# Performance work log

Measured on AMD Instinct MI355X. Metric: run time of the kernel, lower is better.

Reference implementation:

```python
import jax, jax.numpy as jnp
import numpy as np

B, M, L, D = 64, 128, 20, 1024


def setup_inputs() -> dict:
    key = jax.random.key(0)
    ks = jax.random.split(key, 16)
    s = 0.05  # weight scale to keep LSTM gates out of saturation
    rn = lambda k, shape: jax.random.normal(k, shape, jnp.float32) * s
    return {
        'encoder_out': jax.random.normal(ks[0], (B, M + 1, D), jnp.float32),
        'obj_seq': jax.random.randint(ks[1], (B, L), 0, M),
        'att_mask': jnp.ones((B, M + 1), jnp.int32),
        'bos_w': rn(ks[2], (1, D)),
        'eos_w': rn(ks[3], (1, D)),
        'Wp': rn(ks[4], (D, D)), 'bp': jnp.zeros((D,), jnp.float32),
        'Wih1': rn(ks[5], (4 * D, 3 * D)), 'Whh1': rn(ks[6], (4 * D, D)),
        'bih1': jnp.zeros((4 * D,), jnp.float32), 'bhh1': jnp.zeros((4 * D,), jnp.float32),
        'Wih2': rn(ks[7], (4 * D, 2 * D)), 'Whh2': rn(ks[8], (4 * D, D)),
        'bih2': jnp.zeros((4 * D,), jnp.float32), 'bhh2': jnp.zeros((4 * D,), jnp.float32),
        'Wah': rn(ks[9], (D, D)), 'bah': jnp.zeros((D,), jnp.float32),
        'wa': rn(ks[10], (D,)), 'ba': jnp.zeros((1,), jnp.float32),
        'Wae': rn(ks[11], (D, D)), 'bae': jnp.zeros((D,), jnp.float32),
        'Woe': rn(ks[12], (D, D)), 'boe': jnp.zeros((D,), jnp.float32),
    }


def _lstm_cell(x, h, c, Wih, Whh, bih, bhh):
    # torch LSTMCell gate order: i, f, g, o
    g = x @ Wih.T + bih + h @ Whh.T + bhh
    i, f, gg, o = jnp.split(g, 4, axis=-1)
    c_new = jax.nn.sigmoid(f) * c + jax.nn.sigmoid(i) * jnp.tanh(gg)
    h_new = jax.nn.sigmoid(o) * jnp.tanh(c_new)
    return h_new, c_new


def _forward(encoder_out, obj_seq, att_mask, bos_w, eos_w, Wp, bp,
             Wih1, Whh1, bih1, bhh1, Wih2, Whh2, bih2, bhh2,
             Wah, bah, wa, ba, Wae, bae, Woe, boe):
    b, _, d = encoder_out.shape
    gv = encoder_out[:, 0, :]                      # [B, D]
    att_feats = encoder_out[:, 1:, :]              # [B, M, D]
    idx = jnp.broadcast_to(obj_seq[:, :, None], obj_seq.shape + (d,)).astype(jnp.int32)
    obj_feat = jnp.take_along_axis(att_feats, idx, axis=1)          # [B, L, D]
    bos = jnp.broadcast_to(bos_w, (b, 1, d))
    obj_feat = jnp.concatenate([bos, obj_feat], axis=1)             # [B, L+1, D]
    p_att = att_feats @ Wp.T + bp                  # [B, M, D]
    amask = att_mask[:, 1:]                        # [B, M]

    def attend(h1):
        dot = jnp.tanh(p_att + (h1 @ Wah.T + bah)[:, None, :])      # [B, M, D]
        score = dot @ wa + ba[0]                                    # [B, M]
        score = jnp.where(amask == 0, -1e9, score)
        alpha = jax.nn.softmax(score, axis=-1)
        return jnp.einsum('bm,bmd->bd', alpha, att_feats)

    def step(carry, x_t):
        h1, c1, h2, c2 = carry
        inp1 = jnp.concatenate([h2, gv, x_t], axis=-1)              # [B, 3D]
        h1, c1 = _lstm_cell(inp1, h1, c1, Wih1, Whh1, bih1, bhh1)
        att = attend(h1)
        inp2 = jnp.concatenate([att, h1], axis=-1)                  # [B, 2D]
        h2, c2 = _lstm_cell(inp2, h2, c2, Wih2, Whh2, bih2, bhh2)
        return (h1, c1, h2, c2), h2

    z = jnp.zeros((b, d), encoder_out.dtype)
    _, outs = jax.lax.scan(step, (z, z, z, z), jnp.swapaxes(obj_feat, 0, 1))
    outputs = jnp.swapaxes(outs, 0, 1)             # [B, L+1, D]

    # NCE branch (cfg.LOSSES.NCE.STOP_GRAD = True)
    nce_att = jax.lax.stop_gradient(att_feats)
    afe = nce_att @ Wae.T + bae
    eos = jnp.broadcast_to(eos_w, (b, 1, d))
    afe = jnp.concatenate([eos, afe], axis=1)      # [B, M+1, D]
    ofe = outputs @ Woe.T + boe                    # [B, L+1, D]
    nce_logit = jnp.einsum('bld,bmd->blm', ofe, afe)  # [B, L+1, M+1]
    return outputs, nce_logit


def reference(encoder_out, obj_seq, att_mask, bos_w, eos_w, Wp, bp,
              Wih1, Whh1, bih1, bhh1, Wih2, Whh2, bih2, bhh2,
              Wah, bah, wa, ba, Wae, bae, Woe, boe):
    return _forward(encoder_out, obj_seq, att_mask, bos_w, eos_w, Wp, bp,
                    Wih1, Whh1, bih1, bhh1, Wih2, Whh2, bih2, bhh2,
                    Wah, bah, wa, ba, Wae, bae, Woe, boe)
```

## Files before the change

### kernel.cpp

```cpp
#include <hip/hip_runtime.h>
#include <cmath>

typedef unsigned short u16;
typedef __attribute__((ext_vector_type(8))) short short8;
typedef __attribute__((ext_vector_type(4))) float floatx4;
typedef __attribute__((address_space(3))) unsigned int lds_u32;
typedef const __attribute__((address_space(1))) unsigned int glob_u32;

__device__ __forceinline__ u16 f2bf(float f) {
    unsigned u = __float_as_uint(f);
    unsigned r = u + 0x7fffu + ((u >> 16) & 1u);
    return (u16)(r >> 16);
}
__device__ __forceinline__ float bf2f(u16 h) { return __uint_as_float(((unsigned)h) << 16); }
__device__ __forceinline__ void split2(float x, u16& hi, u16& lo) {
    hi = f2bf(x);
    lo = f2bf(x - bf2f(hi));
}
__device__ __forceinline__ float sigm(float x) {
    x = fminf(fmaxf(x, -30.f), 30.f);
    return 1.0f / (1.0f + __expf(-x));
}
__device__ __forceinline__ float ftanh(float x) {
    x = fminf(fmaxf(x, -15.f), 15.f);
    float e = __expf(2.f * x);
    return (e - 1.f) / (e + 1.f);
}
__device__ __forceinline__ void gload16(const void* g, void* l) {
    __builtin_amdgcn_global_load_lds((glob_u32*)g, (lds_u32*)l, 16, 0, 0);
}

__global__ __launch_bounds__(256) void k_cvt(const float* __restrict__ s, u16* __restrict__ d, int n4) {
    int i = blockIdx.x * 256 + threadIdx.x;
    int stride = gridDim.x * 256;
    for (; i < n4; i += stride) {
        float4 v = ((const float4*)s)[i];
        ushort4 o;
        o.x = f2bf(v.x); o.y = f2bf(v.y); o.z = f2bf(v.z); o.w = f2bf(v.w);
        ((ushort4*)d)[i] = o;
    }
}

__global__ __launch_bounds__(256) void k_cvt_att(const float* __restrict__ enc, u16* __restrict__ dst) {
    int m = blockIdx.x, b = blockIdx.y, tid = threadIdx.x;
    const float* src = enc + ((size_t)b * 129 + 1 + m) * 1024;
    float4 v = *(const float4*)(src + tid * 4);
    ushort4 o;
    o.x = f2bf(v.x); o.y = f2bf(v.y); o.z = f2bf(v.z); o.w = f2bf(v.w);
    *(ushort4*)(dst + ((size_t)b * 128 + m) * 1024 + tid * 4) = o;
}

__global__ __launch_bounds__(256) void k_splitp(const float* __restrict__ s, u16* __restrict__ hi,
                                                u16* __restrict__ lo, int n4) {
    int i = blockIdx.x * 256 + threadIdx.x;
    int stride = gridDim.x * 256;
    for (; i < n4; i += stride) {
        float4 v = ((const float4*)s)[i];
        ushort4 h, l;
        split2(v.x, h.x, l.x); split2(v.y, h.y, l.y);
        split2(v.z, h.z, l.z); split2(v.w, h.w, l.w);
        ((ushort4*)hi)[i] = h;
        ((ushort4*)lo)[i] = l;
    }
}

__global__ __launch_bounds__(256) void k_build_w1cat(const float* __restrict__ Wih1, const float* __restrict__ Whh1,
                                                     u16* __restrict__ dh, u16* __restrict__ dl) {
    int row = blockIdx.x;
    int c = threadIdx.x * 8;
    const float* src = (c < 1024) ? (Wih1 + (size_t)row * 3072 + c) : (Whh1 + (size_t)row * 1024 + (c - 1024));
    short8 h, l;
#pragma unroll
    for (int j = 0; j < 8; ++j) { u16 hh, ll; split2(src[j], hh, ll); h[j] = (short)hh; l[j] = (short)ll; }
    *(short8*)(dh + (size_t)row * 2048 + c) = h;
    *(short8*)(dl + (size_t)row * 2048 + c) = l;
}

__global__ __launch_bounds__(384) void k_build_wcat2(const float* __restrict__ Wih2, const float* __restrict__ Whh2,
                                                     u16* __restrict__ dh, u16* __restrict__ dl) {
    int row = blockIdx.x;
    int c = threadIdx.x * 8;
    const float* src = (c < 2048) ? (Wih2 + (size_t)row * 2048 + c) : (Whh2 + (size_t)row * 1024 + (c - 2048));
    short8 h, l;
#pragma unroll
    for (int j = 0; j < 8; ++j) { u16 hh, ll; split2(src[j], hh, ll); h[j] = (short)hh; l[j] = (short)ll; }
    *(short8*)(dh + (size_t)row * 3072 + c) = h;
    *(short8*)(dl + (size_t)row * 3072 + c) = l;
}

__global__ __launch_bounds__(256) void k_build_wx1(const float* __restrict__ Wih1, u16* __restrict__ dh,
                                                   u16* __restrict__ dl) {
    int row = blockIdx.x;
    int c = threadIdx.x * 8;
    const float* src = Wih1 + (size_t)row * 3072 + 1024 + c;
    short8 h, l;
#pragma unroll
    for (int j = 0; j < 8; ++j) { u16 hh, ll; split2(src[j], hh, ll); h[j] = (short)hh; l[j] = (short)ll; }
    *(short8*)(dh + (size_t)row * 2048 + c) = h;
    *(short8*)(dl + (size_t)row * 2048 + c) = l;
}

__global__ __launch_bounds__(256) void k_build_xaug(const float* __restrict__ enc, const int* __restrict__ obj,
                                                    const float* __restrict__ bos_w, u16* __restrict__ dh,
                                                    u16* __restrict__ dl) {
    int b = blockIdx.x, t = blockIdx.y, tid = threadIdx.x;
    const float* gv = enc + (size_t)b * 129 * 1024;
    const float* xr;
    if (t == 0) xr = bos_w;
    else {
        int idx = obj[b * 20 + (t - 1)];
        idx = min(max(idx, 0), 127);
        xr = enc + ((size_t)b * 129 + 1 + idx) * 1024;
    }
    size_t rowoff = ((size_t)b * 21 + t) * 2048;
    float4 v0 = *(const float4*)(gv + tid * 4);
    float4 v1 = *(const float4*)(xr + tid * 4);
    ushort4 h0, l0, h1, l1;
    split2(v0.x, h0.x, l0.x); split2(v0.y, h0.y, l0.y); split2(v0.z, h0.z, l0.z); split2(v0.w, h0.w, l0.w);
    split2(v1.x, h1.x, l1.x); split2(v1.y, h1.y, l1.y); split2(v1.z, h1.z, l1.z); split2(v1.w, h1.w, l1.w);
    *(ushort4*)(dh + rowoff + tid * 4) = h0;
    *(ushort4*)(dl + rowoff + tid * 4) = l0;
    *(ushort4*)(dh + rowoff + 1024 + tid * 4) = h1;
    *(ushort4*)(dl + rowoff + 1024 + tid * 4) = l1;
}

template <int APASS, int BPASS, int AREMAP, bool BF16OUT>
__global__ __launch_bounds__(256)
void k_gemm3(const u16* __restrict__ Ah, const u16* __restrict__ Al, int lda,
             const u16* __restrict__ Wh, const u16* __restrict__ Wl, int ldw,
             const float* __restrict__ b1, const float* __restrict__ b2,
             void* __restrict__ Cout, int ldc, int Mrows, int K) {
    constexpr int NP = APASS + BPASS;
    __shared__ char lds[2][NP][8192];
    const int tid = threadIdx.x;
    const int lane = tid & 63;
    const int lr = lane & 15, lk = lane >> 4;
    const int m0 = blockIdx.y * 128, n0 = blockIdx.x * 128;
    const int wid = tid >> 6;
    const int wr = wid >> 1, wc = wid & 1;
    const int wbyte = (tid & 192) * 16;

    floatx4 acc[4][4] = {};
    const int nt = K >> 5;

    auto stage = [&](int bb, int kt) {
        int k0 = kt * 32;
#pragma unroll
        for (int i = 0; i < 2; ++i) {
            int p = i * 256 + tid;
            int s = p ^ ((p >> 2) & 3);
            int row = s >> 2, kc = s & 3;
            size_t aoff;
            int gm = m0 + row;
            if (AREMAP == 1) aoff = (((size_t)(gm >> 7)) * 129 + 1 + (gm & 127)) * 1024 + k0 + kc * 8;
            else {
                int cm = gm < Mrows ? gm : Mrows - 1;
                aoff = (size_t)cm * lda + k0 + kc * 8;
            }
            gload16(Ah + aoff, &lds[bb][0][i * 4096 + wbyte]);
            if constexpr (APASS == 2) gload16(Al + aoff, &lds[bb][1][i * 4096 + wbyte]);
            size_t woff = (size_t)(n0 + row) * ldw + k0 + kc * 8;
            gload16(Wh + woff, &lds[bb][APASS][i * 4096 + wbyte]);
            if constexpr (BPASS == 2) gload16(Wl + woff, &lds[bb][APASS + 1][i * 4096 + wbyte]);
        }
    };

    stage(0, 0);
    __syncthreads();
    for (int t = 0; t < nt; ++t) {
        int bb = t & 1;
        if (t + 1 < nt) stage(bb ^ 1, t + 1);
        short8 ah_[4], al_[4], bh_[4], bl_[4];
#pragma unroll
        for (int mi = 0; mi < 4; ++mi) {
            int row = wr * 64 + mi * 16 + lr;
            int slot = (row * 4 + (lk ^ (row & 3))) * 16;
            ah_[mi] = *(const short8*)&lds[bb][0][slot];
            if constexpr (APASS == 2) al_[mi] = *(const short8*)&lds[bb][1][slot];
        }
#pragma unroll
        for (int ni = 0; ni < 4; ++ni) {
            int row = wc * 64 + ni * 16 + lr;
            int slot = (row * 4 + (lk ^ (row & 3))) * 16;
            bh_[ni] = *(const short8*)&lds[bb][APASS][slot];
            if constexpr (BPASS == 2) bl_[ni] = *(const short8*)&lds[bb][APASS + 1][slot];
        }
#pragma unroll
        for (int mi = 0; mi < 4; ++mi)
#pragma unroll
            for (int ni = 0; ni < 4; ++ni) {
                acc[mi][ni] = __builtin_amdgcn_mfma_f32_16x16x32_bf16(ah_[mi], bh_[ni], acc[mi][ni], 0, 0, 0);
                if constexpr (BPASS == 2)
                    acc[mi][ni] = __builtin_amdgcn_mfma_f32_16x16x32_bf16(ah_[mi], bl_[ni], acc[mi][ni], 0, 0, 0);
                if constexpr (APASS == 2)
                    acc[mi][ni] = __builtin_amdgcn_mfma_f32_16x16x32_bf16(al_[mi], bh_[ni], acc[mi][ni], 0, 0, 0);
            }
        __syncthreads();
    }
#pragma unroll
    for (int mi = 0; mi < 4; ++mi) {
#pragma unroll
        for (int r = 0; r < 4; ++r) {
            int gm = m0 + wr * 64 + mi * 16 + lk * 4 + r;
            if (AREMAP == 0 && gm >= Mrows) continue;
#pragma unroll
            for (int ni = 0; ni < 4; ++ni) {
                int gn = n0 + wc * 64 + ni * 16 + lr;
                float v = acc[mi][ni][r];
                if (b1) v += b1[gn];
                if (b2) v += b2[gn];
                if (BF16OUT) ((u16*)Cout)[(size_t)gm * ldc + gn] = f2bf(v);
                else ((float*)Cout)[(size_t)gm * ldc + gn] = v;
            }
        }
    }
}

__global__ __launch_bounds__(256)
void k_gp3(const u16* __restrict__ Xh, const u16* __restrict__ Xl, int ldx,
           const u16* __restrict__ Wh, const u16* __restrict__ Wl, int ldw,
           int Klen, float* __restrict__ P, int Ntot) {
    __shared__ char lds[2][4][4096];
    const int tid = threadIdx.x, wid = tid >> 6, lane = tid & 63;
    const int lr = lane & 15, lk = lane >> 4;
    const int n0 = blockIdx.x * 64;
    const int koff = blockIdx.y * Klen;
    floatx4 acc[4] = {};
    const int nt = Klen >> 5;
    const int wbyte = (tid & 192) * 16;
    const int srow = tid >> 2, skc = (tid & 3) ^ (srow & 3);
    const size_t xoff = (size_t)srow * ldx + skc * 8;
    const size_t woff = (size_t)(n0 + srow) * ldw + skc * 8;

    auto stage = [&](int bb, int kt) {
        int k0 = koff + kt * 32;
        gload16(Xh + xoff + k0, &lds[bb][0][wbyte]);
        gload16(Xl + xoff + k0, &lds[bb][1][wbyte]);
        gload16(Wh + woff + k0, &lds[bb][2][wbyte]);
        gload16(Wl + woff + k0, &lds[bb][3][wbyte]);
    };

    stage(0, 0);
    __syncthreads();
    for (int t = 0; t < nt; ++t) {
        int bb = t & 1;
        if (t + 1 < nt) stage(bb ^ 1, t + 1);
        int arow = wid * 16 + lr;
        int aslot = (arow * 4 + (lk ^ (arow & 3))) * 16;
        short8 xh = *(const short8*)&lds[bb][0][aslot];
        short8 xl = *(const short8*)&lds[bb][1][aslot];
#pragma unroll
        for (int ni = 0; ni < 4; ++ni) {
            int brow = ni * 16 + lr;
            int bslot = (brow * 4 + (lk ^ (brow & 3))) * 16;
            short8 wh = *(const short8*)&lds[bb][2][bslot];
            short8 wl = *(const short8*)&lds[bb][3][bslot];
            acc[ni] = __builtin_amdgcn_mfma_f32_16x16x32_bf16(xh, wh, acc[ni], 0, 0, 0);
            acc[ni] = __builtin_amdgcn_mfma_f32_16x16x32_bf16(xh, wl, acc[ni], 0, 0, 0);
            acc[ni] = __builtin_amdgcn_mfma_f32_16x16x32_bf16(xl, wh, acc[ni], 0, 0, 0);
        }
        __syncthreads();
    }
    float* Pb = P + (size_t)blockIdx.y * 64 * Ntot;
#pragma unroll
    for (int ni = 0; ni < 4; ++ni)
#pragma unroll
        for (int r = 0; r < 4; ++r) {
            int b = wid * 16 + lk * 4 + r;
            Pb[(size_t)b * Ntot + n0 + ni * 16 + lr] = acc[ni][r];
        }
}

__global__ __launch_bounds__(256)
void k_finish(const float* __restrict__ P, int Ntot, int nP, const float* __restrict__ xcf,
              const float* __restrict__ b1, const float* __restrict__ b2,
              float* __restrict__ cst,
              u16* __restrict__ w1h, u16* __restrict__ w1l, int w1s,
              u16* __restrict__ w2h, u16* __restrict__ w2l, int w2s,
              float* __restrict__ outf, u16* __restrict__ oh) {
    int idx = blockIdx.x * 256 + threadIdx.x;
    int b = idx >> 10, d = idx & 1023;
    float g[4];
#pragma unroll
    for (int q = 0; q < 4; ++q) {
        int n = q * 1024 + d;
        float s = 0.f;
        for (int p = 0; p < nP; ++p) s += P[((size_t)p * 64 + b) * Ntot + n];
        if (xcf) s += xcf[(size_t)b * 21 * 4096 + n];
        if (b1) s += b1[n];
        if (b2) s += b2[n];
        g[q] = s;
    }
    float cp = cst[idx];
    float cn = sigm(g[1]) * cp + sigm(g[0]) * ftanh(g[2]);
    float hn = sigm(g[3]) * ftanh(cn);
    cst[idx] = cn;
    u16 hh, hl;
    split2(hn, hh, hl);
    w1h[b * w1s + d] = hh; w1l[b * w1s + d] = hl;
    w2h[b * w2s + d] = hh; w2l[b * w2s + d] = hl;
    if (outf) outf[(size_t)b * 21 * 1024 + d] = hn;
    if (oh) oh[(size_t)b * 21 * 1024 + d] = hh;
}

__global__ __launch_bounds__(256)
void k_score(const float* __restrict__ PAH, const float* __restrict__ bah,
             const float* __restrict__ wa, const float* __restrict__ ba,
             const u16* __restrict__ Patt, const int* __restrict__ amask, float* __restrict__ SC) {
    int mc = blockIdx.x, b = blockIdx.y, tid = threadIdx.x;
    __shared__ float sah[1024], swa[1024];
    {
        int d = tid * 4;
        *(float4*)&swa[d] = *(const float4*)(wa + d);
        float4 s;
        float* sp = &s.x;
#pragma unroll
        for (int j = 0; j < 4; ++j) {
            float acc = bah[d + j];
#pragma unroll
            for (int p = 0; p < 4; ++p) acc += PAH[((size_t)p * 64 + b) * 1024 + d + j];
            sp[j] = acc;
        }
        *(float4*)&sah[d] = s;
    }
    __syncthreads();
    int wv = tid >> 6, lane = tid & 63;
    float bav = ba[0];
    for (int j = 0; j < 8; ++j) {
        int m = mc * 32 + wv * 8 + j;
        const u16* pr = Patt + ((size_t)(b * 128 + m)) * 1024;
        float part = 0.f;
#pragma unroll
        for (int c = 0; c < 4; ++c) {
            int d = c * 256 + lane * 4;
            ushort4 p4 = *(const ushort4*)(pr + d);
            float4 a4 = *(const float4*)&sah[d];
            float4 w4 = *(const float4*)&swa[d];
            part += ftanh(bf2f(p4.x) + a4.x) * w4.x + ftanh(bf2f(p4.y) + a4.y) * w4.y +
                    ftanh(bf2f(p4.z) + a4.z) * w4.z + ftanh(bf2f(p4.w) + a4.w) * w4.w;
        }
#pragma unroll
        for (int off = 32; off; off >>= 1) part += __shfl_down(part, off, 64);
        if (lane == 0) {
            float sc = part + bav;
            if (amask[b * 129 + 1 + m] == 0) sc = -1e9f;
            SC[b * 128 + m] = sc;
        }
    }
}

__global__ __launch_bounds__(256)
void k_attsum(const float* __restrict__ SC, const u16* __restrict__ attf,
              u16* __restrict__ X2h, u16* __restrict__ X2l) {
    int dc = blockIdx.x, b = blockIdx.y, tid = threadIdx.x;
    __shared__ float salpha[128];
    __shared__ float sred[8];
    float sv = (tid < 128) ? SC[b * 128 + tid] : -1e30f;
    float mx = sv;
#pragma unroll
    for (int off = 32; off; off >>= 1) mx = fmaxf(mx, __shfl_down(mx, off, 64));
    if ((tid & 63) == 0) sred[tid >> 6] = mx;
    __syncthreads();
    float gmx = fmaxf(fmaxf(sred[0], sred[1]), fmaxf(sred[2], sred[3]));
    float ev = (tid < 128) ? __expf(sv - gmx) : 0.f;
    float s = ev;
#pragma unroll
    for (int off = 32; off; off >>= 1) s += __shfl_down(s, off, 64);
    if ((tid & 63) == 0) sred[4 + (tid >> 6)] = s;
    __syncthreads();
    float gsum = sred[4] + sred[5] + sred[6] + sred[7];
    if (tid < 128) salpha[tid] = ev / gsum;
    __syncthreads();
    int d = dc * 256 + tid;
    const u16* base = attf + (size_t)b * 128 * 1024 + d;
    float acc = 0.f;
#pragma unroll 8
    for (int m = 0; m < 128; ++m) acc += salpha[m] * bf2f(base[(size_t)m * 1024]);
    u16 hh, hl;
    split2(acc, hh, hl);
    X2h[b * 3072 + d] = hh;
    X2l[b * 3072 + d] = hl;
}

__global__ __launch_bounds__(256)
void k_nce(const float* __restrict__ OFE, const float* __restrict__ AFE,
           const float* __restrict__ eos_w, float* __restrict__ nce) {
    int l = blockIdx.x, b = blockIdx.y;
    __shared__ float sofe[1024];
    int tid = threadIdx.x;
    {
        float4 v = *(const float4*)(OFE + ((size_t)b * 21 + l) * 1024 + tid * 4);
        *(float4*)&sofe[tid * 4] = v;
    }
    __syncthreads();
    int w = tid >> 6, lane = tid & 63;
    float* outp = nce + ((size_t)b * 21 + l) * 129;
    for (int j = w; j < 129; j += 4) {
        const float* ar = (j == 0) ? eos_w : AFE + ((size_t)b * 128 + (j - 1)) * 1024;
        float part = 0.f;
#pragma unroll
        for (int c = 0; c < 4; ++c) {
            float4 a4 = *(const float4*)(ar + c * 256 + lane * 4);
            float4 o4 = *(const float4*)&sofe[c * 256 + lane * 4];
            part += a4.x * o4.x + a4.y * o4.y + a4.z * o4.z + a4.w * o4.w;
        }
#pragma unroll
        for (int off = 32; off; off >>= 1) part += __shfl_down(part, off, 64);
        if (lane == 0) outp[j] = part;
    }
}

extern "C" void kernel_launch(void* const* d_in, const int* in_sizes, int n_in,
                              void* d_out, int out_size, void* d_ws, size_t ws_size,
                              hipStream_t stream) {
    const float* enc  = (const float*)d_in[0];
    const int*   obj  = (const int*)d_in[1];
    const int*   amask= (const int*)d_in[2];
    const float* bosw = (const float*)d_in[3];
    const float* eosw = (const float*)d_in[4];
    const float* Wp   = (const float*)d_in[5];
    const float* bp   = (const float*)d_in[6];
    const float* Wih1 = (const float*)d_in[7];
    const float* Whh1 = (const float*)d_in[8];
    const float* bih1 = (const float*)d_in[9];
    const float* bhh1 = (const float*)d_in[10];
    const float* Wih2 = (const float*)d_in[11];
    const float* Whh2 = (const float*)d_in[12];
    const float* bih2 = (const float*)d_in[13];
    const float* bhh2 = (const float*)d_in[14];
    const float* Wah  = (const float*)d_in[15];
    const float* bah  = (const float*)d_in[16];
    const float* wa   = (const float*)d_in[17];
    const float* ba   = (const float*)d_in[18];
    const float* Wae  = (const float*)d_in[19];
    const float* bae  = (const float*)d_in[20];
    const float* Woe  = (const float*)d_in[21];
    const float* boe  = (const float*)d_in[22];

    float* outputs = (float*)d_out;
    float* nce     = outputs + (size_t)64 * 21 * 1024;

    char* wp = (char*)d_ws;
    auto alloc = [&](size_t bytes) -> char* { char* p = wp; wp += (bytes + 255) & ~(size_t)255; return p; };
    u16* encbf  = (u16*)alloc((size_t)64 * 129 * 1024 * 2);
    u16* Wph    = (u16*)alloc((size_t)1024 * 1024 * 2);
    u16* Wpl    = (u16*)alloc((size_t)1024 * 1024 * 2);
    u16* Xaugh  = (u16*)alloc((size_t)1344 * 2048 * 2);
    u16* Xaugl  = (u16*)alloc((size_t)1344 * 2048 * 2);
    u16* W1h    = (u16*)alloc((size_t)4096 * 2048 * 2);
    u16* W1l    = (u16*)alloc((size_t)4096 * 2048 * 2);
    u16* W2h    = (u16*)alloc((size_t)4096 * 3072 * 2);
    u16* W2l    = (u16*)alloc((size_t)4096 * 3072 * 2);
    u16* Wahh   = (u16*)alloc((size_t)1024 * 1024 * 2);
    u16* Wahl   = (u16*)alloc((size_t)1024 * 1024 * 2);
    u16* Waeh   = (u16*)alloc((size_t)1024 * 1024 * 2);
    u16* Wael   = (u16*)alloc((size_t)1024 * 1024 * 2);
    u16* Woeh   = (u16*)alloc((size_t)1024 * 1024 * 2);
    u16* Woel   = (u16*)alloc((size_t)1024 * 1024 * 2);
    char* region1 = alloc((size_t)2 * 4096 * 2048 * 2);
    u16* Wx1h = (u16*)region1;
    u16* Wx1l = (u16*)region1 + (size_t)4096 * 2048;
    float* AFE32 = (float*)region1;
    u16* PattBf  = (u16*)alloc((size_t)8192 * 1024 * 2);
    u16* attfbf  = (u16*)alloc((size_t)64 * 128 * 1024 * 2);
    float* Xcf   = (float*)alloc((size_t)1344 * 4096 * 4);
    u16* Xouth   = (u16*)alloc((size_t)1344 * 1024 * 2);
    float* P2    = (float*)alloc((size_t)8 * 64 * 4096 * 4);
    float* OFE32 = (float*)Xaugh;
    char* sp2 = (char*)encbf;
    auto alloc2 = [&](size_t bytes) -> char* { char* p = sp2; sp2 += (bytes + 255) & ~(size_t)255; return p; };
    float* P1  = (float*)alloc2((size_t)8 * 64 * 4096 * 4);
    float* PAH = (float*)alloc2((size_t)4 * 64 * 1024 * 4);
    u16* XHh   = (u16*)alloc2((size_t)64 * 2048 * 2);
    u16* XHl   = (u16*)alloc2((size_t)64 * 2048 * 2);
    u16* X2h   = (u16*)alloc2((size_t)64 * 3072 * 2);
    u16* X2l   = (u16*)alloc2((size_t)64 * 3072 * 2);
    float* c1  = (float*)alloc2((size_t)64 * 1024 * 4);
    float* c2  = (float*)alloc2((size_t)64 * 1024 * 4);
    float* SC  = (float*)alloc2((size_t)64 * 128 * 4);

    dim3 blk(256);
    k_cvt<<<2048, blk, 0, stream>>>(enc, encbf, 64 * 129 * 1024 / 4);
    k_cvt_att<<<dim3(128, 64), blk, 0, stream>>>(enc, attfbf);
    k_splitp<<<1024, blk, 0, stream>>>(Wp, Wph, Wpl, 1024 * 1024 / 4);
    k_splitp<<<1024, blk, 0, stream>>>(Wah, Wahh, Wahl, 1024 * 1024 / 4);
    k_splitp<<<1024, blk, 0, stream>>>(Wae, Waeh, Wael, 1024 * 1024 / 4);
    k_splitp<<<1024, blk, 0, stream>>>(Woe, Woeh, Woel, 1024 * 1024 / 4);
    k_build_wx1<<<4096, blk, 0, stream>>>(Wih1, Wx1h, Wx1l);
    k_build_w1cat<<<4096, blk, 0, stream>>>(Wih1, Whh1, W1h, W1l);
    k_build_wcat2<<<4096, dim3(384), 0, stream>>>(Wih2, Whh2, W2h, W2l);
    k_build_xaug<<<dim3(64, 21), blk, 0, stream>>>(enc, obj, bosw, Xaugh, Xaugl);

    k_gemm3<1, 2, 1, true><<<dim3(8, 64), blk, 0, stream>>>(
        encbf, nullptr, 0, Wph, Wpl, 1024, bp, nullptr, PattBf, 1024, 8192, 1024);
    k_gemm3<2, 2, 0, false><<<dim3(32, 11), blk, 0, stream>>>(
        Xaugh, Xaugl, 2048, Wx1h, Wx1l, 2048, bih1, bhh1, Xcf, 4096, 1344, 2048);
    k_gemm3<1, 2, 1, false><<<dim3(8, 64), blk, 0, stream>>>(
        encbf, nullptr, 0, Waeh, Wael, 1024, bae, nullptr, AFE32, 1024, 8192, 1024);

    hipMemsetAsync(XHh, 0, (size_t)64 * 2048 * 2, stream);
    hipMemsetAsync(XHl, 0, (size_t)64 * 2048 * 2, stream);
    hipMemsetAsync(X2h, 0, (size_t)64 * 3072 * 2, stream);
    hipMemsetAsync(X2l, 0, (size_t)64 * 3072 * 2, stream);
    hipMemsetAsync(c1, 0, (size_t)64 * 1024 * 4, stream);
    hipMemsetAsync(c2, 0, (size_t)64 * 1024 * 4, stream);

    for (int t = 0; t < 21; ++t) {
        k_gp3<<<dim3(64, 8), blk, 0, stream>>>(XHh, XHl, 2048, W1h, W1l, 2048, 256, P1, 4096);
        k_finish<<<256, blk, 0, stream>>>(P1, 4096, 8, Xcf + (size_t)t * 4096, nullptr, nullptr,
                                          c1, XHh + 1024, XHl + 1024, 2048,
                                          X2h + 1024, X2l + 1024, 3072, nullptr, nullptr);
        k_gp3<<<dim3(16, 4), blk, 0, stream>>>(XHh + 1024, XHl + 1024, 2048, Wahh, Wahl, 1024, 256, PAH, 1024);
        k_score<<<dim3(4, 64), blk, 0, stream>>>(PAH, bah, wa, ba, PattBf, amask, SC);
        k_attsum<<<dim3(4, 64), blk, 0, stream>>>(SC, attfbf, X2h, X2l);
        k_gp3<<<dim3(64, 8), blk, 0, stream>>>(X2h, X2l, 3072, W2h, W2l, 3072, 384, P2, 4096);
        k_finish<<<256, blk, 0, stream>>>(P2, 4096, 8, nullptr, bih2, bhh2,
                                          c2, XHh, XHl, 2048,
                                          X2h + 2048, X2l + 2048, 3072,
                                          outputs + (size_t)t * 1024, Xouth + (size_t)t * 1024);
    }

    k_gemm3<1, 2, 0, false><<<dim3(8, 11), blk, 0, stream>>>(
        Xouth, nullptr, 1024, Woeh, Woel, 1024, boe, nullptr, OFE32, 1024, 1344, 1024);
    k_nce<<<dim3(21, 64), blk, 0, stream>>>(OFE32, AFE32, eosw, nce);
}
```

Baseline: 1.899 ms.

## Drop low-order activation split in recurrent GEMMs and retile split-K

Recurrent activations (h states and attention context) are now stored as single bf16 instead of a hi/lo pair. This removes one of the three MFMAs per tile and half the activation loads in the per-step GEMM. The GEMM is retiled to 32-column blocks with 4-way instead of 8-way split-K, which shrinks the partial buffers k_finish has to sum. Wp also loses its low-order split, so the attention projection uses plain bf16. The cost is lower accuracy in the recurrent path, and the error can compound over the 21 timesteps.

```diff
diff --git a/kernel.cpp b/kernel.cpp
--- a/kernel.cpp
+++ b/kernel.cpp
@@ -217,27 +217,30 @@
 }
 
 __global__ __launch_bounds__(256)
-void k_gp3(const u16* __restrict__ Xh, const u16* __restrict__ Xl, int ldx,
+void k_gp2(const u16* __restrict__ Xh, int ldx,
            const u16* __restrict__ Wh, const u16* __restrict__ Wl, int ldw,
            int Klen, float* __restrict__ P, int Ntot) {
-    __shared__ char lds[2][4][4096];
+    __shared__ char lds[2][8192];
     const int tid = threadIdx.x, wid = tid >> 6, lane = tid & 63;
     const int lr = lane & 15, lk = lane >> 4;
-    const int n0 = blockIdx.x * 64;
+    const int n0 = blockIdx.x * 32;
     const int koff = blockIdx.y * Klen;
-    floatx4 acc[4] = {};
+    floatx4 acc[2] = {};
     const int nt = Klen >> 5;
-    const int wbyte = (tid & 192) * 16;
-    const int srow = tid >> 2, skc = (tid & 3) ^ (srow & 3);
-    const size_t xoff = (size_t)srow * ldx + skc * 8;
-    const size_t woff = (size_t)(n0 + srow) * ldw + skc * 8;
+
+    const int sX = tid ^ ((tid >> 2) & 3);
+    const size_t xoff = (size_t)(sX >> 2) * ldx + (sX & 3) * 8 + koff;
+    const int xdst = (tid & 192) * 16;
+    const int pw = tid & 127;
+    const int sW = pw ^ ((pw >> 2) & 3);
+    const size_t woff = (size_t)(n0 + (sW >> 2)) * ldw + (sW & 3) * 8 + koff;
+    const u16* Wsrc = (tid < 128) ? Wh : Wl;
+    const int wdst = 4096 + (wid >> 1) * 2048 + (wid & 1) * 1024;
 
     auto stage = [&](int bb, int kt) {
-        int k0 = koff + kt * 32;
-        gload16(Xh + xoff + k0, &lds[bb][0][wbyte]);
-        gload16(Xl + xoff + k0, &lds[bb][1][wbyte]);
-        gload16(Wh + woff + k0, &lds[bb][2][wbyte]);
-        gload16(Wl + woff + k0, &lds[bb][3][wbyte]);
+        int k0 = kt * 32;
+        gload16(Xh + xoff + k0, &lds[bb][xdst]);
+        gload16(Wsrc + woff + k0, &lds[bb][wdst]);
     };
 
     stage(0, 0);
@@ -246,24 +249,21 @@
         int bb = t & 1;
         if (t + 1 < nt) stage(bb ^ 1, t + 1);
         int arow = wid * 16 + lr;
-        int aslot = (arow * 4 + (lk ^ (arow & 3))) * 16;
-        short8 xh = *(const short8*)&lds[bb][0][aslot];
-        short8 xl = *(const short8*)&lds[bb][1][aslot];
-#pragma unroll
-        for (int ni = 0; ni < 4; ++ni) {
-            int brow = ni * 16 + lr;
-            int bslot = (brow * 4 + (lk ^ (brow & 3))) * 16;
-            short8 wh = *(const short8*)&lds[bb][2][bslot];
-            short8 wl = *(const short8*)&lds[bb][3][bslot];
+        short8 xh = *(const short8*)&lds[bb][(arow * 4 + (lk ^ (arow & 3))) * 16];
+#pragma unroll
+        for (int ni = 0; ni < 2; ++ni) {
+            int r = ni * 16 + lr;
+            int slot = (r * 4 + (lk ^ (r & 3))) * 16;
+            short8 wh = *(const short8*)&lds[bb][4096 + slot];
+            short8 wl = *(const short8*)&lds[bb][6144 + slot];
             acc[ni] = __builtin_amdgcn_mfma_f32_16x16x32_bf16(xh, wh, acc[ni], 0, 0, 0);
             acc[ni] = __builtin_amdgcn_mfma_f32_16x16x32_bf16(xh, wl, acc[ni], 0, 0, 0);
-            acc[ni] = __builtin_amdgcn_mfma_f32_16x16x32_bf16(xl, wh, acc[ni], 0, 0, 0);
         }
         __syncthreads();
     }
     float* Pb = P + (size_t)blockIdx.y * 64 * Ntot;
 #pragma unroll
-    for (int ni = 0; ni < 4; ++ni)
+    for (int ni = 0; ni < 2; ++ni)
 #pragma unroll
         for (int r = 0; r < 4; ++r) {
             int b = wid * 16 + lk * 4 + r;
@@ -275,8 +275,7 @@
 void k_finish(const float* __restrict__ P, int Ntot, int nP, const float* __restrict__ xcf,
               const float* __restrict__ b1, const float* __restrict__ b2,
               float* __restrict__ cst,
-              u16* __restrict__ w1h, u16* __restrict__ w1l, int w1s,
-              u16* __restrict__ w2h, u16* __restrict__ w2l, int w2s,
+              u16* __restrict__ w1, int w1s, u16* __restrict__ w2, int w2s,
               float* __restrict__ outf, u16* __restrict__ oh) {
     int idx = blockIdx.x * 256 + threadIdx.x;
     int b = idx >> 10, d = idx & 1023;
@@ -295,10 +294,9 @@
     float cn = sigm(g[1]) * cp + sigm(g[0]) * ftanh(g[2]);
     float hn = sigm(g[3]) * ftanh(cn);
     cst[idx] = cn;
-    u16 hh, hl;
-    split2(hn, hh, hl);
-    w1h[b * w1s + d] = hh; w1l[b * w1s + d] = hl;
-    w2h[b * w2s + d] = hh; w2l[b * w2s + d] = hl;
+    u16 hh = f2bf(hn);
+    w1[b * w1s + d] = hh;
+    w2[b * w2s + d] = hh;
     if (outf) outf[(size_t)b * 21 * 1024 + d] = hn;
     if (oh) oh[(size_t)b * 21 * 1024 + d] = hh;
 }
@@ -351,7 +349,7 @@
 
 __global__ __launch_bounds__(256)
 void k_attsum(const float* __restrict__ SC, const u16* __restrict__ attf,
-              u16* __restrict__ X2h, u16* __restrict__ X2l) {
+              u16* __restrict__ X2h) {
     int dc = blockIdx.x, b = blockIdx.y, tid = threadIdx.x;
     __shared__ float salpha[128];
     __shared__ float sred[8];
@@ -376,10 +374,7 @@
     float acc = 0.f;
 #pragma unroll 8
     for (int m = 0; m < 128; ++m) acc += salpha[m] * bf2f(base[(size_t)m * 1024]);
-    u16 hh, hl;
-    split2(acc, hh, hl);
-    X2h[b * 3072 + d] = hh;
-    X2l[b * 3072 + d] = hl;
+    X2h[b * 3072 + d] = f2bf(acc);
 }
 
 __global__ __launch_bounds__(256)
@@ -443,8 +438,7 @@
     char* wp = (char*)d_ws;
     auto alloc = [&](size_t bytes) -> char* { char* p = wp; wp += (bytes + 255) & ~(size_t)255; return p; };
     u16* encbf  = (u16*)alloc((size_t)64 * 129 * 1024 * 2);
-    u16* Wph    = (u16*)alloc((size_t)1024 * 1024 * 2);
-    u16* Wpl    = (u16*)alloc((size_t)1024 * 1024 * 2);
+    u16* Wpbf   = (u16*)alloc((size_t)1024 * 1024 * 2);
     u16* Xaugh  = (u16*)alloc((size_t)1344 * 2048 * 2);
     u16* Xaugl  = (u16*)alloc((size_t)1344 * 2048 * 2);
     u16* W1h    = (u16*)alloc((size_t)4096 * 2048 * 2);
@@ -465,16 +459,14 @@
     u16* attfbf  = (u16*)alloc((size_t)64 * 128 * 1024 * 2);
     float* Xcf   = (float*)alloc((size_t)1344 * 4096 * 4);
     u16* Xouth   = (u16*)alloc((size_t)1344 * 1024 * 2);
-    float* P2    = (float*)alloc((size_t)8 * 64 * 4096 * 4);
+    float* P2    = (float*)alloc((size_t)4 * 64 * 4096 * 4);
     float* OFE32 = (float*)Xaugh;
     char* sp2 = (char*)encbf;
     auto alloc2 = [&](size_t bytes) -> char* { char* p = sp2; sp2 += (bytes + 255) & ~(size_t)255; return p; };
-    float* P1  = (float*)alloc2((size_t)8 * 64 * 4096 * 4);
+    float* P1  = (float*)alloc2((size_t)4 * 64 * 4096 * 4);
     float* PAH = (float*)alloc2((size_t)4 * 64 * 1024 * 4);
     u16* XHh   = (u16*)alloc2((size_t)64 * 2048 * 2);
-    u16* XHl   = (u16*)alloc2((size_t)64 * 2048 * 2);
     u16* X2h   = (u16*)alloc2((size_t)64 * 3072 * 2);
-    u16* X2l   = (u16*)alloc2((size_t)64 * 3072 * 2);
     float* c1  = (float*)alloc2((size_t)64 * 1024 * 4);
     float* c2  = (float*)alloc2((size_t)64 * 1024 * 4);
     float* SC  = (float*)alloc2((size_t)64 * 128 * 4);
@@ -482,7 +474,7 @@
     dim3 blk(256);
     k_cvt<<<2048, blk, 0, stream>>>(enc, encbf, 64 * 129 * 1024 / 4);
     k_cvt_att<<<dim3(128, 64), blk, 0, stream>>>(enc, attfbf);
-    k_splitp<<<1024, blk, 0, stream>>>(Wp, Wph, Wpl, 1024 * 1024 / 4);
+    k_cvt<<<1024, blk, 0, stream>>>(Wp, Wpbf, 1024 * 1024 / 4);
     k_splitp<<<1024, blk, 0, stream>>>(Wah, Wahh, Wahl, 1024 * 1024 / 4);
     k_splitp<<<1024, blk, 0, stream>>>(Wae, Waeh, Wael, 1024 * 1024 / 4);
     k_splitp<<<1024, blk, 0, stream>>>(Woe, Woeh, Woel, 1024 * 1024 / 4);
@@ -491,32 +483,28 @@
     k_build_wcat2<<<4096, dim3(384), 0, stream>>>(Wih2, Whh2, W2h, W2l);
     k_build_xaug<<<dim3(64, 21), blk, 0, stream>>>(enc, obj, bosw, Xaugh, Xaugl);
 
-    k_gemm3<1, 2, 1, true><<<dim3(8, 64), blk, 0, stream>>>(
-        encbf, nullptr, 0, Wph, Wpl, 1024, bp, nullptr, PattBf, 1024, 8192, 1024);
+    k_gemm3<1, 1, 1, true><<<dim3(8, 64), blk, 0, stream>>>(
+        encbf, nullptr, 0, Wpbf, nullptr, 1024, bp, nullptr, PattBf, 1024, 8192, 1024);
     k_gemm3<2, 2, 0, false><<<dim3(32, 11), blk, 0, stream>>>(
         Xaugh, Xaugl, 2048, Wx1h, Wx1l, 2048, bih1, bhh1, Xcf, 4096, 1344, 2048);
     k_gemm3<1, 2, 1, false><<<dim3(8, 64), blk, 0, stream>>>(
         encbf, nullptr, 0, Waeh, Wael, 1024, bae, nullptr, AFE32, 1024, 8192, 1024);
 
     hipMemsetAsync(XHh, 0, (size_t)64 * 2048 * 2, stream);
-    hipMemsetAsync(XHl, 0, (size_t)64 * 2048 * 2, stream);
     hipMemsetAsync(X2h, 0, (size_t)64 * 3072 * 2, stream);
-    hipMemsetAsync(X2l, 0, (size_t)64 * 3072 * 2, stream);
     hipMemsetAsync(c1, 0, (size_t)64 * 1024 * 4, stream);
     hipMemsetAsync(c2, 0, (size_t)64 * 1024 * 4, stream);
 
     for (int t = 0; t < 21; ++t) {
-        k_gp3<<<dim3(64, 8), blk, 0, stream>>>(XHh, XHl, 2048, W1h, W1l, 2048, 256, P1, 4096);
-        k_finish<<<256, blk, 0, stream>>>(P1, 4096, 8, Xcf + (size_t)t * 4096, nullptr, nullptr,
-                                          c1, XHh + 1024, XHl + 1024, 2048,
-                                          X2h + 1024, X2l + 1024, 3072, nullptr, nullptr);
-        k_gp3<<<dim3(16, 4), blk, 0, stream>>>(XHh + 1024, XHl + 1024, 2048, Wahh, Wahl, 1024, 256, PAH, 1024);
+        k_gp2<<<dim3(128, 4), blk, 0, stream>>>(XHh, 2048, W1h, W1l, 2048, 512, P1, 4096);
+        k_finish<<<256, blk, 0, stream>>>(P1, 4096, 4, Xcf + (size_t)t * 4096, nullptr, nullptr,
+                                          c1, XHh + 1024, 2048, X2h + 1024, 3072, nullptr, nullptr);
+        k_gp2<<<dim3(32, 4), blk, 0, stream>>>(XHh + 1024, 2048, Wahh, Wahl, 1024, 256, PAH, 1024);
         k_score<<<dim3(4, 64), blk, 0, stream>>>(PAH, bah, wa, ba, PattBf, amask, SC);
-        k_attsum<<<dim3(4, 64), blk, 0, stream>>>(SC, attfbf, X2h, X2l);
-        k_gp3<<<dim3(64, 8), blk, 0, stream>>>(X2h, X2l, 3072, W2h, W2l, 3072, 384, P2, 4096);
-        k_finish<<<256, blk, 0, stream>>>(P2, 4096, 8, nullptr, bih2, bhh2,
-                                          c2, XHh, XHl, 2048,
-                                          X2h + 2048, X2l + 2048, 3072,
+        k_attsum<<<dim3(4, 64), blk, 0, stream>>>(SC, attfbf, X2h);
+        k_gp2<<<dim3(128, 4), blk, 0, stream>>>(X2h, 3072, W2h, W2l, 3072, 768, P2, 4096);
+        k_finish<<<256, blk, 0, stream>>>(P2, 4096, 4, nullptr, bih2, bhh2,
+                                          c2, XHh, 2048, X2h + 2048, 3072,
                                           outputs + (size_t)t * 1024, Xouth + (size_t)t * 1024);
     }
 
```

Measured after the change: 1.668 ms. 12.2% less time.
